# Kernel optimization log

Measured on AMD Instinct MI355X. Metric: run time of the kernel, lower is better.

Reference implementation:

```python
import jax, jax.numpy as jnp
import numpy as np
from functools import partial

N_NODES = 100000
N_REL = 3
N_EDGES = 200000
IN_F = 128
HID_F = 128
OUT_F = 128
N_QUERY = 4096


def _graph_conv(x, es, ed, W, b, n_nodes):
    """DGL GraphConv with norm='both': D_dst^{-1/2} A D_src^{-1/2} X W + b.
    es/ed: [E] int edge endpoints, x: [N, d_in], W: [d_in, d_out], b: [d_out]."""
    ones = jnp.ones(es.shape[0], dtype=x.dtype)
    out_deg = jnp.clip(jax.ops.segment_sum(ones, es, num_segments=n_nodes), 1.0)
    in_deg = jnp.clip(jax.ops.segment_sum(ones, ed, num_segments=n_nodes), 1.0)
    # transform first (dense GEMM), then gather -> scatter-add over dst
    y = (x * jax.lax.rsqrt(out_deg)[:, None]) @ W          # [N, d_out]
    msg = y[es]                                            # [E, d_out] gather
    agg = jax.ops.segment_sum(msg, ed, num_segments=n_nodes)  # [N, d_out]
    return agg * jax.lax.rsqrt(in_deg)[:, None] + b


def _hetero_layer(x, e_src, e_dst, W, b, n_nodes):
    # HeteroGraphConv(aggregate='sum'): sum per-relation GraphConv outputs.
    out = _graph_conv(x, e_src[0], e_dst[0], W[0], b[0], n_nodes)
    for r in range(1, e_src.shape[0]):
        out = out + _graph_conv(x, e_src[r], e_dst[r], W[r], b[r], n_nodes)
    return out


def setup_inputs() -> dict:
    key = jax.random.key(0)
    ks = jax.random.split(key, 9)
    s = 1.0 / np.sqrt(IN_F)
    return {
        "emb": jax.random.normal(ks[0], (N_NODES, IN_F), jnp.float32),
        "W1": jax.random.normal(ks[1], (N_REL, IN_F, HID_F), jnp.float32) * s,
        "b1": jnp.zeros((N_REL, HID_F), jnp.float32),
        "W2": jax.random.normal(ks[2], (N_REL, HID_F, OUT_F), jnp.float32) * s,
        "b2": jnp.zeros((N_REL, OUT_F), jnp.float32),
        "e_src": jax.random.randint(ks[3], (N_REL, N_EDGES), 0, N_NODES, jnp.int32),
        "e_dst": jax.random.randint(ks[4], (N_REL, N_EDGES), 0, N_NODES, jnp.int32),
        "src": jax.random.randint(ks[5], (N_QUERY,), 0, N_NODES, jnp.int32),
        "dst": jax.random.randint(ks[6], (N_QUERY,), 0, N_NODES, jnp.int32),
    }


def reference(emb, W1, b1, W2, b2, e_src, e_dst, src, dst):
    n = emb.shape[0]
    h = jnp.tanh(_hetero_layer(emb, e_src, e_dst, W1, b1, n))
    h = jnp.tanh(_hetero_layer(h, e_src, e_dst, W2, b2, n))
    return (h[src], h[dst])
```

## Files before the change

### kernel.cpp

```cpp
#include <hip/hip_runtime.h>
#include <stdint.h>

#define NN 100000
#define NREL 3
#define NE 200000
#define F 128
#define NQ 4096

#define NBUCK (NREL * NN)
#define NCB ((NBUCK + 255) / 256)
#define CH_BLOCKS 64
#define CH_CHUNK ((NREL * NE) / CH_BLOCKS)

#define WCVT_N (2 * NREL * F * F)
#define A1 (WCVT_N + 256)
#define A2 (A1 + NN * F / 8)
#define A3 (A2 + NREL * NN)
#define A4 (A3 + NCB)
#define A5 (A4 + 2 * NQ)
#define A6 (A5 + NN)
#define PREP_N (A6 + 1)

typedef float fx4 __attribute__((ext_vector_type(4)));
typedef unsigned short u16x8 __attribute__((ext_vector_type(8)));
typedef __bf16 bf16x8 __attribute__((ext_vector_type(8)));

__device__ __forceinline__ unsigned short f2bf(float f) {
  uint32_t u = __builtin_bit_cast(uint32_t, f);
  uint32_t r = u + 0x7FFFu + ((u >> 16) & 1u);
  return (unsigned short)(r >> 16);
}
__device__ __forceinline__ float bf2f(unsigned short u) {
  return __builtin_bit_cast(float, (uint32_t)u << 16);
}
__device__ __forceinline__ int rel_of(int i) {
  return (i >= 2 * NE) ? 2 : (i >= NE ? 1 : 0);
}

__global__ void prep_kernel(const float* __restrict__ W1, const float* __restrict__ W2,
                            const float* __restrict__ b1, const float* __restrict__ b2,
                            const float* __restrict__ emb,
                            const int* __restrict__ qsrc, const int* __restrict__ qdst,
                            unsigned short* __restrict__ Wtb, float* __restrict__ bsum,
                            unsigned short* __restrict__ xb,
                            int* __restrict__ cnt_src, int* __restrict__ chist,
                            int* __restrict__ qnode, int* __restrict__ mark,
                            int* __restrict__ cursor) {
  int i = blockIdx.x * blockDim.x + threadIdx.x;
  if (i < WCVT_N) {
    int l = i / (NREL * F * F);
    int rem = i % (NREL * F * F);
    int r = rem / (F * F);
    int nk = rem % (F * F);
    int n = nk >> 7, k = nk & 127;
    const float* W = l ? W2 : W1;
    Wtb[i] = f2bf(W[r * F * F + k * F + n]);
  } else if (i < A1) {
    int t = i - WCVT_N;
    int l = t >> 7, f = t & 127;
    const float* b = l ? b2 : b1;
    bsum[l * F + f] = b[f] + b[F + f] + b[2 * F + f];
  } else if (i < A2) {
    int j = i - A1;
    const float* p = emb + (size_t)j * 8;
    unsigned short tmp[8];
#pragma unroll
    for (int e = 0; e < 8; ++e) tmp[e] = f2bf(p[e]);
    *reinterpret_cast<u16x8*>(xb + (size_t)j * 8) = *reinterpret_cast<u16x8*>(tmp);
  } else if (i < A3) {
    cnt_src[i - A2] = 0;
  } else if (i < A4) {
    chist[i - A3] = 0;
  } else if (i < A5) {
    int m = i - A4;
    qnode[m] = (m < NQ) ? qsrc[m] : qdst[m - NQ];
  } else if (i < A6) {
    mark[i - A5] = 0;
  } else if (i < PREP_N) {
    *cursor = 0;
  }
}

__global__ __launch_bounds__(256) void coarseH_kernel(const int* __restrict__ es,
                                                      const int* __restrict__ ed,
                                                      int* __restrict__ H,
                                                      int* __restrict__ chist,
                                                      int* __restrict__ cnt_src) {
  __shared__ int h[NCB];
  int t = threadIdx.x, blk = blockIdx.x;
  for (int j = t; j < NCB; j += 256) h[j] = 0;
  __syncthreads();
  int lo = blk * CH_CHUNK;
  for (int i = lo + t; i < lo + CH_CHUNK; i += 256) {
    int r = rel_of(i);
    int b = r * NN + ed[i];
    atomicAdd(&h[b >> 8], 1);
    atomicAdd(&cnt_src[r * NN + es[i]], 1);
  }
  __syncthreads();
  for (int j = t; j < NCB; j += 256) {
    int v = h[j];
    H[j * CH_BLOCKS + blk] = v;
    if (v) atomicAdd(&chist[j], v);
  }
}

__global__ __launch_bounds__(256) void cscan_kernel(const int* __restrict__ chist,
                                                    int* __restrict__ cstart) {
  int t = threadIdx.x, lane = t & 63, w = t >> 6;
  int v[5];
  int s = 0;
#pragma unroll
  for (int k = 0; k < 5; ++k) {
    int i = t * 5 + k;
    v[k] = (i < NCB) ? chist[i] : 0;
    s += v[k];
  }
  int sc = s;
#pragma unroll
  for (int d = 1; d < 64; d <<= 1) {
    int o = __shfl_up(sc, d);
    if (lane >= d) sc += o;
  }
  __shared__ int wt[4];
  if (lane == 63) wt[w] = sc;
  __syncthreads();
  int woff = 0;
#pragma unroll
  for (int ww = 0; ww < 3; ++ww) woff += (ww < w) ? wt[ww] : 0;
  int excl = woff + sc - s;
#pragma unroll
  for (int k = 0; k < 5; ++k) {
    int i = t * 5 + k;
    if (i < NCB) { cstart[i] = excl; excl += v[k]; }
  }
}

__global__ __launch_bounds__(256) void hbase_kernel(const int* __restrict__ H,
                                                    const int* __restrict__ cstart,
                                                    int* __restrict__ Hbase) {
  int t = threadIdx.x, lane = t & 63;
  int bin = blockIdx.x * 4 + (t >> 6);
  int v = H[bin * CH_BLOCKS + lane];
  int sc = v;
#pragma unroll
  for (int d = 1; d < 64; d <<= 1) {
    int o = __shfl_up(sc, d);
    if (lane >= d) sc += o;
  }
  Hbase[bin * CH_BLOCKS + lane] = cstart[bin] + sc - v;
}

__global__ __launch_bounds__(256) void cscatter_kernel(const int* __restrict__ es,
                                                       const int* __restrict__ ed,
                                                       const int* __restrict__ Hbase,
                                                       int* __restrict__ etmp) {
  __shared__ int cur[NCB];
  int t = threadIdx.x, blk = blockIdx.x;
  for (int j = t; j < NCB; j += 256) cur[j] = Hbase[j * CH_BLOCKS + blk];
  __syncthreads();
  int lo = blk * CH_CHUNK;
  for (int i = lo + t; i < lo + CH_CHUNK; i += 256) {
    int b = rel_of(i) * NN + ed[i];
    int pos = atomicAdd(&cur[b >> 8], 1);
    etmp[pos] = (es[i] << 8) | (b & 255);
  }
}

__global__ __launch_bounds__(256) void fine_kernel(const int* __restrict__ etmp,
                                                   const int* __restrict__ cstart,
                                                   const int* __restrict__ chist,
                                                   const int* __restrict__ cnt_src,
                                                   int2* __restrict__ scb,
                                                   int2* __restrict__ epay) {
  const int cb = blockIdx.x;
  const int t = threadIdx.x, lane = t & 63, w = t >> 6;
  const int cs = cstart[cb], cc = chist[cb];
  __shared__ int fcnt[256], fexcl[256], fcur[256];
  fcnt[t] = 0;
  fcur[t] = 0;
  __syncthreads();
  for (int i = t; i < cc; i += 256) atomicAdd(&fcnt[etmp[cs + i] & 255], 1);
  __syncthreads();
  int val = fcnt[t];
  int sc = val;
#pragma unroll
  for (int d = 1; d < 64; d <<= 1) {
    int o = __shfl_up(sc, d);
    if (lane >= d) sc += o;
  }
  __shared__ int wt[4];
  if (lane == 63) wt[w] = sc;
  __syncthreads();
  int woff = 0;
#pragma unroll
  for (int ww = 0; ww < 3; ++ww) woff += (ww < w) ? wt[ww] : 0;
  fexcl[t] = woff + sc - val;
  int b = cb * 256 + t;
  if (b < NBUCK) scb[b] = make_int2(cs + fexcl[t], val);
  __syncthreads();
  for (int i = t; i < cc; i += 256) {
    int e = etmp[cs + i];
    int f = e & 255;
    int src = ((unsigned)e) >> 8;
    int r = (cb * 256 + f) / NN;
    float wgt = rsqrtf((float)cnt_src[r * NN + src]) * rsqrtf((float)fcnt[f]);
    int pos = cs + fexcl[f] + atomicAdd(&fcur[f], 1);
    epay[pos] = make_int2(src, __builtin_bit_cast(int, wgt));
  }
}

__global__ void mark_kernel(const int* __restrict__ qnode, const int2* __restrict__ scb,
                            const int2* __restrict__ epay, int* __restrict__ mark) {
  int m = blockIdx.x * blockDim.x + threadIdx.x;
  if (m >= 2 * NQ) return;
  int n = qnode[m];
#pragma unroll
  for (int r = 0; r < NREL; ++r) {
    int2 meta = scb[r * NN + n];
    for (int i = 0; i < meta.y; ++i) mark[epay[meta.x + i].x] = 1;
  }
}

__global__ __launch_bounds__(256) void compact_kernel(const int* __restrict__ mark,
                                                      int* __restrict__ list,
                                                      int* __restrict__ cursor) {
  int t = threadIdx.x, lane = t & 63, w = t >> 6;
  int base = blockIdx.x * 1024 + t * 4;
  int loc[4];
  int cnt = 0;
#pragma unroll
  for (int k = 0; k < 4; ++k) {
    int i = base + k;
    if (i < NN && mark[i]) { loc[cnt] = i; ++cnt; }
  }
  int sc = cnt;
#pragma unroll
  for (int d = 1; d < 64; d <<= 1) {
    int o = __shfl_up(sc, d);
    if (lane >= d) sc += o;
  }
  int texcl = sc - cnt;
  __shared__ int wt[4];
  __shared__ int bb;
  if (lane == 63) wt[w] = sc;
  __syncthreads();
  if (t == 0) {
    int tot = wt[0] + wt[1] + wt[2] + wt[3];
    bb = atomicAdd(cursor, tot);
    int a = 0;
#pragma unroll
    for (int ww = 0; ww < 4; ++ww) { int c = wt[ww]; wt[ww] = a; a += c; }
  }
  __syncthreads();
  int p = bb + wt[w] + texcl;
  for (int k = 0; k < cnt; ++k) list[p + k] = loc[k];
}

__global__ __launch_bounds__(256) void aggz_kernel(const unsigned short* __restrict__ X,
                                                   const int2* __restrict__ scb,
                                                   const int2* __restrict__ epay,
                                                   const int* __restrict__ nmap,
                                                   const int* __restrict__ cntp,
                                                   unsigned short* __restrict__ Z,
                                                   int Mcap, int Ms) {
  const int count = cntp ? *cntp : Mcap;
  const int r = blockIdx.y;
  const int t = threadIdx.x;
  const int lane = t & 63;
  const int m = blockIdx.x * 16 + (t >> 6) * 4 + (lane >> 4);
  const int j = lane & 15;
  if (m >= count) return;
  int n = nmap ? nmap[m] : m;
  int2 meta = scb[r * NN + n];
  const int2* ep = epay + meta.x;
  const int c = meta.y;

  float ps[8];
#pragma unroll
  for (int k = 0; k < 8; ++k) ps[k] = 0.f;

  int i = 0;
  for (; i + 2 <= c; i += 2) {
    int2 p0 = ep[i], p1 = ep[i + 1];
    float w0 = __builtin_bit_cast(float, p0.y);
    float w1 = __builtin_bit_cast(float, p1.y);
    u16x8 v0 = *reinterpret_cast<const u16x8*>(X + ((size_t)p0.x << 7) + j * 8);
    u16x8 v1 = *reinterpret_cast<const u16x8*>(X + ((size_t)p1.x << 7) + j * 8);
#pragma unroll
    for (int k = 0; k < 8; ++k)
      ps[k] = fmaf(bf2f(v1[k]), w1, fmaf(bf2f(v0[k]), w0, ps[k]));
  }
  if (i < c) {
    int2 p0 = ep[i];
    float w0 = __builtin_bit_cast(float, p0.y);
    u16x8 v0 = *reinterpret_cast<const u16x8*>(X + ((size_t)p0.x << 7) + j * 8);
#pragma unroll
    for (int k = 0; k < 8; ++k) ps[k] = fmaf(bf2f(v0[k]), w0, ps[k]);
  }

  unsigned short tmp[8];
#pragma unroll
  for (int k = 0; k < 8; ++k) tmp[k] = f2bf(ps[k]);
  *reinterpret_cast<u16x8*>(Z + (((size_t)r * Ms + m) << 7) + j * 8) =
      *reinterpret_cast<u16x8*>(tmp);
}

#define GBM 128
__global__ __launch_bounds__(512) void gemmp_kernel(const unsigned short* __restrict__ Z,
                                                    const unsigned short* __restrict__ Wt3,
                                                    const float* __restrict__ bsum,
                                                    const int* __restrict__ omap,
                                                    const int* __restrict__ cntp,
                                                    void* __restrict__ outp,
                                                    int M, int Ms, int out_f32) {
  const int count = cntp ? *cntp : M;
  const int m0 = blockIdx.x * GBM;
  if (m0 >= count) return;
  __shared__ unsigned short Abuf[2][GBM * F];
  const int t = threadIdx.x;
  const int lane = t & 63, w = t >> 6;
  const int wm = w >> 2, wn = w & 3;
  const int r0 = lane & 15, kq = lane >> 4;

  fx4 acc[4][2];
#pragma unroll
  for (int mt = 0; mt < 4; ++mt)
#pragma unroll
    for (int nt = 0; nt < 2; ++nt) acc[mt][nt] = (fx4){0.f, 0.f, 0.f, 0.f};

  {
    const unsigned short* Zr = Z + (size_t)m0 * F;
#pragma unroll
    for (int i = 0; i < 4; ++i) {
      int slot = i * 512 + t;
      int row = slot >> 4, s = slot & 15;
      __builtin_amdgcn_global_load_lds(
          (const __attribute__((address_space(1))) uint32_t*)(
              Zr + ((size_t)row << 7) + ((s ^ (row & 7)) << 3)),
          (__attribute__((address_space(3))) uint32_t*)&Abuf[0][slot * 8], 16, 0, 0);
    }
  }
  __syncthreads();

  int cur = 0;
  for (int r = 0; r < NREL; ++r) {
    bf16x8 bfrag[2][4];
    const unsigned short* Wt = Wt3 + (size_t)r * F * F;
#pragma unroll
    for (int nt = 0; nt < 2; ++nt)
#pragma unroll
      for (int kb = 0; kb < 4; ++kb)
        bfrag[nt][kb] = __builtin_bit_cast(bf16x8,
            *reinterpret_cast<const u16x8*>(
                Wt + (wn * 32 + nt * 16 + r0) * F + (4 * kb + kq) * 8));

    if (r + 1 < NREL) {
      const unsigned short* Zr = Z + ((size_t)(r + 1) * Ms + m0) * F;
#pragma unroll
      for (int i = 0; i < 4; ++i) {
        int slot = i * 512 + t;
        int row = slot >> 4, s = slot & 15;
        __builtin_amdgcn_global_load_lds(
            (const __attribute__((address_space(1))) uint32_t*)(
                Zr + ((size_t)row << 7) + ((s ^ (row & 7)) << 3)),
            (__attribute__((address_space(3))) uint32_t*)&Abuf[cur ^ 1][slot * 8],
            16, 0, 0);
      }
    }

#pragma unroll
    for (int kb = 0; kb < 4; ++kb) {
      const int cs = ((kb * 4 + kq) ^ (r0 & 7)) * 8;
      bf16x8 a[4];
#pragma unroll
      for (int mt = 0; mt < 4; ++mt)
        a[mt] = __builtin_bit_cast(bf16x8,
            *reinterpret_cast<const u16x8*>(&Abuf[cur][(wm * 64 + mt * 16 + r0) * F + cs]));
#pragma unroll
      for (int mt = 0; mt < 4; ++mt)
#pragma unroll
        for (int nt = 0; nt < 2; ++nt)
          acc[mt][nt] = __builtin_amdgcn_mfma_f32_16x16x32_bf16(a[mt], bfrag[nt][kb],
                                                                acc[mt][nt], 0, 0, 0);
    }

    __syncthreads();
    cur ^= 1;
  }

#pragma unroll
  for (int mt = 0; mt < 4; ++mt) {
    const int rbase = m0 + wm * 64 + mt * 16 + kq * 4;
#pragma unroll
    for (int nt = 0; nt < 2; ++nt) {
      int col = wn * 32 + nt * 16 + r0;
      float bb = bsum[col];
#pragma unroll
      for (int reg = 0; reg < 4; ++reg) {
        int gm = rbase + reg;
        if (gm < count) {
          float v = tanhf(acc[mt][nt][reg] + bb);
          if (omap) {
            ((unsigned short*)outp)[(size_t)omap[gm] * F + col] = f2bf(v);
          } else if (out_f32) {
            ((float*)outp)[(size_t)gm * F + col] = v;
          } else {
            ((unsigned short*)outp)[(size_t)gm * F + col] = f2bf(v);
          }
        }
      }
    }
  }
}

extern "C" void kernel_launch(void* const* d_in, const int* in_sizes, int n_in,
                              void* d_out, int out_size, void* d_ws, size_t ws_size,
                              hipStream_t stream) {
  const float* emb = (const float*)d_in[0];
  const float* W1  = (const float*)d_in[1];
  const float* b1  = (const float*)d_in[2];
  const float* W2  = (const float*)d_in[3];
  const float* b2  = (const float*)d_in[4];
  const int* e_src = (const int*)d_in[5];
  const int* e_dst = (const int*)d_in[6];
  const int* qsrc  = (const int*)d_in[7];
  const int* qdst  = (const int*)d_in[8];
  float* out = (float*)d_out;

  const int MS1 = ((NN + GBM - 1) / GBM) * GBM;
  const int MQ  = 2 * NQ;

  char* p = (char*)d_ws;
  size_t off = 0;
  auto take = [&](size_t n) { void* q = p + off; off = (off + n + 255) & ~(size_t)255; return q; };
  int* cnt_src = (int*)take((size_t)NREL * NN * 4);
  int* chist   = (int*)take((size_t)NCB * 4);
  int* cstart  = (int*)take((size_t)NCB * 4);
  int* H       = (int*)take((size_t)NCB * CH_BLOCKS * 4);
  int* Hbase   = (int*)take((size_t)NCB * CH_BLOCKS * 4);
  int* etmp    = (int*)take((size_t)NREL * NE * 4);
  int2* scb    = (int2*)take((size_t)NBUCK * 8);
  int2* epay   = (int2*)take((size_t)NREL * NE * 8);
  unsigned short* Wtb = (unsigned short*)take(2ull * NREL * F * F * 2);
  float* bsum  = (float*)take(2ull * F * 4);
  int* qnode   = (int*)take((size_t)MQ * 4);
  int* mark    = (int*)take((size_t)NN * 4);
  int* list    = (int*)take((size_t)NN * 4 + 4);
  int* cursor  = (int*)take(4);
  unsigned short* Xb  = (unsigned short*)take((size_t)NN * F * 2);
  unsigned short* Xb2 = (unsigned short*)take((size_t)NN * F * 2);
  unsigned short* Z   = (unsigned short*)take((size_t)NREL * MS1 * F * 2);

  prep_kernel<<<(PREP_N + 255) / 256, 256, 0, stream>>>(
      W1, W2, b1, b2, emb, qsrc, qdst, Wtb, bsum, Xb, cnt_src, chist, qnode, mark, cursor);
  coarseH_kernel<<<CH_BLOCKS, 256, 0, stream>>>(e_src, e_dst, H, chist, cnt_src);
  cscan_kernel<<<1, 256, 0, stream>>>(chist, cstart);
  hbase_kernel<<<NCB / 4, 256, 0, stream>>>(H, cstart, Hbase);
  cscatter_kernel<<<CH_BLOCKS, 256, 0, stream>>>(e_src, e_dst, Hbase, etmp);
  fine_kernel<<<NCB, 256, 0, stream>>>(etmp, cstart, chist, cnt_src, scb, epay);
  mark_kernel<<<(MQ + 255) / 256, 256, 0, stream>>>(qnode, scb, epay, mark);
  compact_kernel<<<(NN + 1023) / 1024, 256, 0, stream>>>(mark, list, cursor);

  dim3 ag1((NN + 15) / 16, NREL);
  aggz_kernel<<<ag1, 256, 0, stream>>>(Xb, scb, epay, list, cursor, Z, NN, MS1);
  gemmp_kernel<<<MS1 / GBM, 512, 0, stream>>>(Z, Wtb, bsum, list, cursor, Xb2, MS1, MS1, 0);

  dim3 ag2((MQ + 15) / 16, NREL);
  aggz_kernel<<<ag2, 256, 0, stream>>>(Xb2, scb, epay, qnode, nullptr, Z, MQ, MQ);
  gemmp_kernel<<<MQ / GBM, 512, 0, stream>>>(
      Z, Wtb + (size_t)NREL * F * F, bsum + F, nullptr, nullptr, out, MQ, MQ, 1);
}
```

Measured before the change: 163.0 us.

## Replace global source-degree atomics with bucketed counting sort and widen histogram grid

Source-degree counting no longer uses global atomics on a 300K-entry array. Sources are binned through the same two-level coarse/fine counting sort used for destinations, then counted in shared memory. The coarse histogram and scatter passes grow from 64 to 512 blocks, so the per-bin column sums are now computed in a separate reduction kernel instead of with global atomics. This adds an extra 2.4MB scratch write and read plus two more launches, but is meant to remove contended global atomics and expose more parallelism in the sort phase.

Measured after the change: 153.2 us. 1.06x faster.

```diff
diff --git a/kernel.cpp b/kernel.cpp
--- a/kernel.cpp
+++ b/kernel.cpp
@@ -9,17 +9,15 @@
 
 #define NBUCK (NREL * NN)
 #define NCB ((NBUCK + 255) / 256)
-#define CH_BLOCKS 64
-#define CH_CHUNK ((NREL * NE) / CH_BLOCKS)
+#define CH_BLOCKS 512
+#define CH_CHUNK ((NREL * NE + CH_BLOCKS - 1) / CH_BLOCKS)
 
 #define WCVT_N (2 * NREL * F * F)
 #define A1 (WCVT_N + 256)
 #define A2 (A1 + NN * F / 8)
-#define A3 (A2 + NREL * NN)
-#define A4 (A3 + NCB)
-#define A5 (A4 + 2 * NQ)
-#define A6 (A5 + NN)
-#define PREP_N (A6 + 1)
+#define A3 (A2 + 2 * NQ)
+#define A4 (A3 + NN)
+#define PREP_N (A4 + 1)
 
 typedef float fx4 __attribute__((ext_vector_type(4)));
 typedef unsigned short u16x8 __attribute__((ext_vector_type(8)));
@@ -43,7 +41,6 @@
                             const int* __restrict__ qsrc, const int* __restrict__ qdst,
                             unsigned short* __restrict__ Wtb, float* __restrict__ bsum,
                             unsigned short* __restrict__ xb,
-                            int* __restrict__ cnt_src, int* __restrict__ chist,
                             int* __restrict__ qnode, int* __restrict__ mark,
                             int* __restrict__ cursor) {
   int i = blockIdx.x * blockDim.x + threadIdx.x;
@@ -68,45 +65,62 @@
     for (int e = 0; e < 8; ++e) tmp[e] = f2bf(p[e]);
     *reinterpret_cast<u16x8*>(xb + (size_t)j * 8) = *reinterpret_cast<u16x8*>(tmp);
   } else if (i < A3) {
-    cnt_src[i - A2] = 0;
+    int m = i - A2;
+    qnode[m] = (m < NQ) ? qsrc[m] : qdst[m - NQ];
   } else if (i < A4) {
-    chist[i - A3] = 0;
-  } else if (i < A5) {
-    int m = i - A4;
-    qnode[m] = (m < NQ) ? qsrc[m] : qdst[m - NQ];
-  } else if (i < A6) {
-    mark[i - A5] = 0;
+    mark[i - A3] = 0;
   } else if (i < PREP_N) {
     *cursor = 0;
   }
 }
 
-__global__ __launch_bounds__(256) void coarseH_kernel(const int* __restrict__ es,
-                                                      const int* __restrict__ ed,
-                                                      int* __restrict__ H,
-                                                      int* __restrict__ chist,
-                                                      int* __restrict__ cnt_src) {
-  __shared__ int h[NCB];
+__global__ __launch_bounds__(256) void coarseHH_kernel(const int* __restrict__ es,
+                                                       const int* __restrict__ ed,
+                                                       int* __restrict__ Hd,
+                                                       int* __restrict__ Hs) {
+  __shared__ int hd[NCB], hs[NCB];
   int t = threadIdx.x, blk = blockIdx.x;
-  for (int j = t; j < NCB; j += 256) h[j] = 0;
+  for (int j = t; j < NCB; j += 256) { hd[j] = 0; hs[j] = 0; }
   __syncthreads();
   int lo = blk * CH_CHUNK;
-  for (int i = lo + t; i < lo + CH_CHUNK; i += 256) {
+  int hi = min(lo + CH_CHUNK, NREL * NE);
+  for (int i = lo + t; i < hi; i += 256) {
     int r = rel_of(i);
-    int b = r * NN + ed[i];
-    atomicAdd(&h[b >> 8], 1);
-    atomicAdd(&cnt_src[r * NN + es[i]], 1);
+    atomicAdd(&hd[(r * NN + ed[i]) >> 8], 1);
+    atomicAdd(&hs[(r * NN + es[i]) >> 8], 1);
   }
   __syncthreads();
   for (int j = t; j < NCB; j += 256) {
-    int v = h[j];
-    H[j * CH_BLOCKS + blk] = v;
-    if (v) atomicAdd(&chist[j], v);
-  }
-}
-
-__global__ __launch_bounds__(256) void cscan_kernel(const int* __restrict__ chist,
-                                                    int* __restrict__ cstart) {
+    Hd[j * CH_BLOCKS + blk] = hd[j];
+    Hs[j * CH_BLOCKS + blk] = hs[j];
+  }
+}
+
+__global__ __launch_bounds__(256) void hsum_kernel(const int* __restrict__ Hd,
+                                                   const int* __restrict__ Hs,
+                                                   int* __restrict__ chist_d,
+                                                   int* __restrict__ chist_s) {
+  int t = threadIdx.x, lane = t & 63;
+  int ws = blockIdx.x * 4 + (t >> 6);
+  if (ws >= 2 * NCB) return;
+  const int* H = (ws < NCB) ? Hd : Hs;
+  int bin = (ws < NCB) ? ws : ws - NCB;
+  int s = 0;
+#pragma unroll
+  for (int k = 0; k < 8; ++k) s += H[bin * CH_BLOCKS + lane * 8 + k];
+#pragma unroll
+  for (int d = 1; d < 64; d <<= 1) s += __shfl_xor(s, d);
+  if (lane == 0) {
+    if (ws < NCB) chist_d[bin] = s; else chist_s[bin] = s;
+  }
+}
+
+__global__ __launch_bounds__(256) void cscan_kernel(const int* __restrict__ chist_d,
+                                                    const int* __restrict__ chist_s,
+                                                    int* __restrict__ cstart_d,
+                                                    int* __restrict__ cstart_s) {
+  const int* chist = blockIdx.x ? chist_s : chist_d;
+  int* cstart = blockIdx.x ? cstart_s : cstart_d;
   int t = threadIdx.x, lane = t & 63, w = t >> 6;
   int v[5];
   int s = 0;
@@ -136,35 +150,79 @@
   }
 }
 
-__global__ __launch_bounds__(256) void hbase_kernel(const int* __restrict__ H,
-                                                    const int* __restrict__ cstart,
-                                                    int* __restrict__ Hbase) {
+__global__ __launch_bounds__(256) void hbase_kernel(const int* __restrict__ Hd,
+                                                    const int* __restrict__ Hs,
+                                                    const int* __restrict__ cstart_d,
+                                                    const int* __restrict__ cstart_s,
+                                                    int* __restrict__ Hbase_d,
+                                                    int* __restrict__ Hbase_s) {
+  const int* H = blockIdx.y ? Hs : Hd;
+  const int* cstart = blockIdx.y ? cstart_s : cstart_d;
+  int* Hbase = blockIdx.y ? Hbase_s : Hbase_d;
   int t = threadIdx.x, lane = t & 63;
   int bin = blockIdx.x * 4 + (t >> 6);
-  int v = H[bin * CH_BLOCKS + lane];
-  int sc = v;
+  int v[8];
+  int s = 0;
+#pragma unroll
+  for (int k = 0; k < 8; ++k) {
+    v[k] = H[bin * CH_BLOCKS + lane * 8 + k];
+    s += v[k];
+  }
+  int sc = s;
 #pragma unroll
   for (int d = 1; d < 64; d <<= 1) {
     int o = __shfl_up(sc, d);
     if (lane >= d) sc += o;
   }
-  Hbase[bin * CH_BLOCKS + lane] = cstart[bin] + sc - v;
+  int run = cstart[bin] + sc - s;
+#pragma unroll
+  for (int k = 0; k < 8; ++k) {
+    Hbase[bin * CH_BLOCKS + lane * 8 + k] = run;
+    run += v[k];
+  }
 }
 
 __global__ __launch_bounds__(256) void cscatter_kernel(const int* __restrict__ es,
                                                        const int* __restrict__ ed,
-                                                       const int* __restrict__ Hbase,
-                                                       int* __restrict__ etmp) {
-  __shared__ int cur[NCB];
+                                                       const int* __restrict__ Hbase_d,
+                                                       const int* __restrict__ Hbase_s,
+                                                       int* __restrict__ etmp_d,
+                                                       int* __restrict__ etmp_s) {
+  __shared__ int cur_d[NCB], cur_s[NCB];
   int t = threadIdx.x, blk = blockIdx.x;
-  for (int j = t; j < NCB; j += 256) cur[j] = Hbase[j * CH_BLOCKS + blk];
+  for (int j = t; j < NCB; j += 256) {
+    cur_d[j] = Hbase_d[j * CH_BLOCKS + blk];
+    cur_s[j] = Hbase_s[j * CH_BLOCKS + blk];
+  }
   __syncthreads();
   int lo = blk * CH_CHUNK;
-  for (int i = lo + t; i < lo + CH_CHUNK; i += 256) {
-    int b = rel_of(i) * NN + ed[i];
-    int pos = atomicAdd(&cur[b >> 8], 1);
-    etmp[pos] = (es[i] << 8) | (b & 255);
-  }
+  int hi = min(lo + CH_CHUNK, NREL * NE);
+  for (int i = lo + t; i < hi; i += 256) {
+    int r = rel_of(i);
+    int s = es[i], d = ed[i];
+    int bd = r * NN + d;
+    int pos = atomicAdd(&cur_d[bd >> 8], 1);
+    etmp_d[pos] = (s << 8) | (bd & 255);
+    int bs = r * NN + s;
+    int pos_s = atomicAdd(&cur_s[bs >> 8], 1);
+    etmp_s[pos_s] = bs & 255;
+  }
+}
+
+__global__ __launch_bounds__(256) void srccount_kernel(const int* __restrict__ etmp_s,
+                                                       const int* __restrict__ cstart_s,
+                                                       const int* __restrict__ chist_s,
+                                                       int* __restrict__ cnt_src) {
+  const int cb = blockIdx.x;
+  const int t = threadIdx.x;
+  const int cs = cstart_s[cb], cc = chist_s[cb];
+  __shared__ int fcnt[256];
+  fcnt[t] = 0;
+  __syncthreads();
+  for (int i = t; i < cc; i += 256) atomicAdd(&fcnt[etmp_s[cs + i]], 1);
+  __syncthreads();
+  int b = cb * 256 + t;
+  if (b < NBUCK) cnt_src[b] = fcnt[t];
 }
 
 __global__ __launch_bounds__(256) void fine_kernel(const int* __restrict__ etmp,
@@ -434,31 +492,42 @@
   char* p = (char*)d_ws;
   size_t off = 0;
   auto take = [&](size_t n) { void* q = p + off; off = (off + n + 255) & ~(size_t)255; return q; };
-  int* cnt_src = (int*)take((size_t)NREL * NN * 4);
-  int* chist   = (int*)take((size_t)NCB * 4);
-  int* cstart  = (int*)take((size_t)NCB * 4);
-  int* H       = (int*)take((size_t)NCB * CH_BLOCKS * 4);
-  int* Hbase   = (int*)take((size_t)NCB * CH_BLOCKS * 4);
-  int* etmp    = (int*)take((size_t)NREL * NE * 4);
-  int2* scb    = (int2*)take((size_t)NBUCK * 8);
-  int2* epay   = (int2*)take((size_t)NREL * NE * 8);
+  int* cnt_src  = (int*)take((size_t)NREL * NN * 4);
+  int* chist_d  = (int*)take((size_t)NCB * 4);
+  int* chist_s  = (int*)take((size_t)NCB * 4);
+  int* cstart_d = (int*)take((size_t)NCB * 4);
+  int* cstart_s = (int*)take((size_t)NCB * 4);
+  int* Hd       = (int*)take((size_t)NCB * CH_BLOCKS * 4);
+  int* Hs       = (int*)take((size_t)NCB * CH_BLOCKS * 4);
+  int* Hbase_d  = (int*)take((size_t)NCB * CH_BLOCKS * 4);
+  int* Hbase_s  = (int*)take((size_t)NCB * CH_BLOCKS * 4);
+  int* etmp_d   = (int*)take((size_t)NREL * NE * 4);
+  int* etmp_s   = (int*)take((size_t)NREL * NE * 4);
+  int2* scb     = (int2*)take((size_t)NBUCK * 8);
+  int2* epay    = (int2*)take((size_t)NREL * NE * 8);
   unsigned short* Wtb = (unsigned short*)take(2ull * NREL * F * F * 2);
-  float* bsum  = (float*)take(2ull * F * 4);
-  int* qnode   = (int*)take((size_t)MQ * 4);
-  int* mark    = (int*)take((size_t)NN * 4);
-  int* list    = (int*)take((size_t)NN * 4 + 4);
-  int* cursor  = (int*)take(4);
+  float* bsum   = (float*)take(2ull * F * 4);
+  int* qnode    = (int*)take((size_t)MQ * 4);
+  int* mark     = (int*)take((size_t)NN * 4);
+  int* list     = (int*)take((size_t)NN * 4 + 4);
+  int* cursor   = (int*)take(4);
   unsigned short* Xb  = (unsigned short*)take((size_t)NN * F * 2);
   unsigned short* Xb2 = (unsigned short*)take((size_t)NN * F * 2);
   unsigned short* Z   = (unsigned short*)take((size_t)NREL * MS1 * F * 2);
 
   prep_kernel<<<(PREP_N + 255) / 256, 256, 0, stream>>>(
-      W1, W2, b1, b2, emb, qsrc, qdst, Wtb, bsum, Xb, cnt_src, chist, qnode, mark, cursor);
-  coarseH_kernel<<<CH_BLOCKS, 256, 0, stream>>>(e_src, e_dst, H, chist, cnt_src);
-  cscan_kernel<<<1, 256, 0, stream>>>(chist, cstart);
-  hbase_kernel<<<NCB / 4, 256, 0, stream>>>(H, cstart, Hbase);
-  cscatter_kernel<<<CH_BLOCKS, 256, 0, stream>>>(e_src, e_dst, Hbase, etmp);
-  fine_kernel<<<NCB, 256, 0, stream>>>(etmp, cstart, chist, cnt_src, scb, epay);
+      W1, W2, b1, b2, emb, qsrc, qdst, Wtb, bsum, Xb, qnode, mark, cursor);
+  coarseHH_kernel<<<CH_BLOCKS, 256, 0, stream>>>(e_src, e_dst, Hd, Hs);
+  hsum_kernel<<<(2 * NCB + 3) / 4, 256, 0, stream>>>(Hd, Hs, chist_d, chist_s);
+  cscan_kernel<<<2, 256, 0, stream>>>(chist_d, chist_s, cstart_d, cstart_s);
+  {
+    dim3 hb(NCB / 4, 2);
+    hbase_kernel<<<hb, 256, 0, stream>>>(Hd, Hs, cstart_d, cstart_s, Hbase_d, Hbase_s);
+  }
+  cscatter_kernel<<<CH_BLOCKS, 256, 0, stream>>>(e_src, e_dst, Hbase_d, Hbase_s,
+                                                 etmp_d, etmp_s);
+  srccount_kernel<<<NCB, 256, 0, stream>>>(etmp_s, cstart_s, chist_s, cnt_src);
+  fine_kernel<<<NCB, 256, 0, stream>>>(etmp_d, cstart_d, chist_d, cnt_src, scb, epay);
   mark_kernel<<<(MQ + 255) / 256, 256, 0, stream>>>(qnode, scb, epay, mark);
   compact_kernel<<<(NN + 1023) / 1024, 256, 0, stream>>>(mark, list, cursor);
 
```
